# Optimization experiments

Measured on AMD Instinct MI355X. Metric: run time of the kernel, lower is better.

The kernel has to match this reference:

```python
import jax, jax.numpy as jnp
import numpy as np

M0, M1, G = 10.0, 10.0, 10.0  # masses and gravity (hard-coded in the torch module)


def _phi_single(xs):
    # xs: (4,) cartesian positions of the two pendulum bobs
    c1 = xs[0] ** 2 + xs[1] ** 2 - 1.0
    c2 = (xs[0] - xs[2]) ** 2 + (xs[1] - xs[3]) ** 2 - 1.0
    return jnp.stack([c1, c2])  # (2,)


def _potential_single(xs):
    return M0 * G * xs[1] + M1 * G * xs[3]


def setup_inputs() -> dict:
    key = jax.random.key(0)
    bs = 2_097_152
    coords = jax.random.normal(key, (bs, 8), dtype=jnp.float32)
    t = jnp.zeros((1,), dtype=jnp.float32)
    return {"t": t, "coords": coords}


def reference(t, coords):
    x, v = jnp.split(coords, 2, axis=-1)  # each (bs, 4)

    Minv = jnp.diag(1.0 / jnp.array([M0, M0, M1, M1], dtype=coords.dtype))  # (4,4)

    # Jacobian of constraints: phi_q (bs, 2, 4)
    phi_q = jax.vmap(jax.jacfwd(_phi_single))(x)

    # phi_qq = d/dx (phi_q(x) @ v): (bs, 2, 4)
    def _phiq_v(xs, vs):
        return jax.jacfwd(_phi_single)(xs) @ vs  # (2,)

    phi_qq = jax.vmap(jax.jacfwd(_phiq_v), in_axes=(0, 0))(x, v)

    # F = -dV/dx: (bs, 4)
    F = -jax.vmap(jax.grad(_potential_single))(x)

    phiq_Minv = jnp.einsum('bij,jk->bik', phi_q, Minv)        # (bs, 2, 4)
    L = jnp.einsum('bik,bjk->bij', phiq_Minv, phi_q)          # (bs, 2, 2)
    R = (jnp.einsum('bik,bk->bi', phiq_Minv, F)
         + jnp.einsum('bik,bk->bi', phi_qq, v))[..., None]    # (bs, 2, 1)

    lam = jnp.linalg.solve(L, R)                              # (bs, 2, 1)

    a_R = F - jnp.einsum('bik,bi->bk', phi_q, lam[..., 0])    # (bs, 4)
    a = jnp.einsum('jk,bk->bj', Minv, a_R)                    # (bs, 4)

    return jnp.concatenate([v, a], axis=-1)
```

## Files before the change

kernel.cpp:

```cpp
#include <hip/hip_runtime.h>


typedef float f32x4 __attribute__((ext_vector_type(4)));

__device__ __forceinline__ float det2x2(float a, float d, float b, float c) {
  float w = b * c;
  float e = fmaf(b, c, -w);
  float f = fmaf(a, d, -w);
  return f - e;
}

__global__ __launch_bounds__(256) void pendulum_dae_kernel(
    const float* __restrict__ coords, float* __restrict__ out, int n4) {
  int g = blockIdx.x * blockDim.x + threadIdx.x;
  if (g >= n4) return;

  const f32x4* __restrict__ in4 = (const f32x4*)coords;
  f32x4 mine = in4[g];

  f32x4 other;
  other.x = __shfl_xor(mine.x, 1);
  other.y = __shfl_xor(mine.y, 1);
  other.z = __shfl_xor(mine.z, 1);
  other.w = __shfl_xor(mine.w, 1);

  const bool haveX = ((g & 1) == 0);
  f32x4 xv = haveX ? mine : other;
  f32x4 vv = haveX ? other : mine;

  float x0 = xv.x, x1 = xv.y, x2 = xv.z, x3 = xv.w;
  float v0 = vv.x, v1 = vv.y, v2 = vv.z, v3 = vv.w;

  float da = x0 - x2, db = x1 - x3;
  float dv0 = v0 - v2, dv1 = v1 - v3;

  float L00 = 0.4f * fmaf(x0, x0, x1 * x1);
  float L01 = 0.4f * fmaf(x0, da, x1 * db);
  float L11 = 0.8f * fmaf(da, da, db * db);

  float R1 = fmaf(-20.0f, x1, 2.0f * fmaf(v0, v0, v1 * v1));
  float R2 = 2.0f * fmaf(dv0, dv0, dv1 * dv1);

  float det  = det2x2(L00, L11, L01, L01);
  float num1 = det2x2(L11, R1, L01, R2);
  float num2 = det2x2(L00, R2, L01, R1);
  float inv = 1.0f / det;
  float lam1 = num1 * inv;
  float lam2 = num2 * inv;

  float aR0 = -2.0f * fmaf(x0, lam1, da * lam2);
  float aR1 = fmaf(-2.0f, fmaf(x1, lam1, db * lam2), -100.0f);
  float aR2 = 2.0f * da * lam2;
  float aR3 = fmaf(2.0f * db, lam2, -100.0f);

  f32x4 av;
  av.x = 0.1f * aR0;
  av.y = 0.1f * aR1;
  av.z = 0.1f * aR2;
  av.w = 0.1f * aR3;

  f32x4 res = haveX ? vv : av;
  f32x4* __restrict__ out4 = (f32x4*)out;
  out4[g] = res;
}

extern "C" void kernel_launch(void* const* d_in, const int* in_sizes, int n_in,
                              void* d_out, int out_size, void* d_ws,
                              size_t ws_size, hipStream_t stream) {
  const float* coords = (const float*)d_in[1];
  float* out = (float*)d_out;
  int n4 = in_sizes[1] / 4;
  int block = 256;
  int grid = (n4 + block - 1) / block;
  pendulum_dae_kernel<<<grid, block, 0, stream>>>(coords, out, n4);
}
```

Measured before the change: 112.6 us.

## Process eight strided elements per thread with batched loads

Each thread now handles eight grid-strided float4 elements, issuing all loads before computing and storing, and the grid shrinks by the same factor. The aim is more outstanding memory requests per thread and less per-thread launch overhead on a bandwidth-bound kernel. The cost is fewer resident waves and more registers. The tail path puts the lane shuffle under a bounds check, which could diverge when sizes are not multiples of the chunk.

```diff
diff --git a/kernel.cpp b/kernel.cpp
--- a/kernel.cpp
+++ b/kernel.cpp
@@ -2,6 +2,8 @@
 
 
 typedef float f32x4 __attribute__((ext_vector_type(4)));
+
+#define UNROLL 8
 
 __device__ __forceinline__ float det2x2(float a, float d, float b, float c) {
   float w = b * c;
@@ -10,21 +12,13 @@
   return f - e;
 }
 
-__global__ __launch_bounds__(256) void pendulum_dae_kernel(
-    const float* __restrict__ coords, float* __restrict__ out, int n4) {
-  int g = blockIdx.x * blockDim.x + threadIdx.x;
-  if (g >= n4) return;
-
-  const f32x4* __restrict__ in4 = (const f32x4*)coords;
-  f32x4 mine = in4[g];
-
+__device__ __forceinline__ f32x4 solve_one(f32x4 mine, bool haveX) {
   f32x4 other;
   other.x = __shfl_xor(mine.x, 1);
   other.y = __shfl_xor(mine.y, 1);
   other.z = __shfl_xor(mine.z, 1);
   other.w = __shfl_xor(mine.w, 1);
 
-  const bool haveX = ((g & 1) == 0);
   f32x4 xv = haveX ? mine : other;
   f32x4 vv = haveX ? other : mine;
 
@@ -59,9 +53,32 @@
   av.z = 0.1f * aR2;
   av.w = 0.1f * aR3;
 
-  f32x4 res = haveX ? vv : av;
+  return haveX ? vv : av;
+}
+
+__global__ __launch_bounds__(256) void pendulum_dae_kernel(
+    const float* __restrict__ coords, float* __restrict__ out, int n4) {
+  const int stride = gridDim.x * blockDim.x;
+  const int g0 = blockIdx.x * blockDim.x + threadIdx.x;
+  const bool haveX = ((g0 & 1) == 0);
+
+  const f32x4* __restrict__ in4 = (const f32x4*)coords;
   f32x4* __restrict__ out4 = (f32x4*)out;
-  out4[g] = res;
+
+  if (g0 + (UNROLL - 1) * stride < n4) {
+    f32x4 mine[UNROLL];
+#pragma unroll
+    for (int j = 0; j < UNROLL; ++j) mine[j] = in4[g0 + j * stride];
+#pragma unroll
+    for (int j = 0; j < UNROLL; ++j) {
+      out4[g0 + j * stride] = solve_one(mine[j], haveX);
+    }
+  } else {
+    for (int j = 0; j < UNROLL; ++j) {
+      int g = g0 + j * stride;
+      if (g < n4) out4[g] = solve_one(in4[g], haveX);
+    }
+  }
 }
 
 extern "C" void kernel_launch(void* const* d_in, const int* in_sizes, int n_in,
@@ -71,6 +88,7 @@
   float* out = (float*)d_out;
   int n4 = in_sizes[1] / 4;
   int block = 256;
-  int grid = (n4 + block - 1) / block;
+  int per_block = block * UNROLL;
+  int grid = (n4 + per_block - 1) / per_block;
   pendulum_dae_kernel<<<grid, block, 0, stream>>>(coords, out, n4);
 }
```

After: 116.9 us. 1.04x slower.
